# Performance work log

Measured on AMD Instinct MI355X. Metric: run time of the kernel, lower is better.

Reference implementation:

```python
import jax, jax.numpy as jnp
import numpy as np

B, Q, C, N, H, W = 2, 4096, 256, 6, 64, 96
HEADS, POINTS = 8, 4


def _grid_sample(img, grid):
    # img: [G, C, H, W]; grid: [G, P, 2] in [-1,1]
    # bilinear, align_corners=False, padding_mode='zeros' (matches F.grid_sample)
    G, Cc, Hh, Ww = img.shape
    gx = (grid[..., 0] + 1.0) * (Ww / 2.0) - 0.5
    gy = (grid[..., 1] + 1.0) * (Hh / 2.0) - 0.5
    x0f = jnp.floor(gx)
    y0f = jnp.floor(gy)
    wx = (gx - x0f)[:, None, :]
    wy = (gy - y0f)[:, None, :]
    x0 = x0f.astype(jnp.int32)
    y0 = y0f.astype(jnp.int32)
    flat = img.reshape(G, Cc, Hh * Ww)

    def gather(xi, yi):
        valid = ((xi >= 0) & (xi < Ww) & (yi >= 0) & (yi < Hh))
        idx = jnp.clip(yi, 0, Hh - 1) * Ww + jnp.clip(xi, 0, Ww - 1)
        v = jnp.take_along_axis(flat, idx[:, None, :], axis=2)  # [G,C,P]
        return v * valid[:, None, :].astype(img.dtype)

    v00 = gather(x0, y0)
    v01 = gather(x0 + 1, y0)
    v10 = gather(x0, y0 + 1)
    v11 = gather(x0 + 1, y0 + 1)
    return (v00 * (1 - wx) * (1 - wy) + v01 * wx * (1 - wy)
            + v10 * (1 - wx) * wy + v11 * wx * wy)


def setup_inputs() -> dict:
    key = jax.random.key(0)
    ks = jax.random.split(key, 12)
    query = jax.random.normal(ks[0], (B, Q, C), dtype=jnp.float32)
    query_coords = jax.random.uniform(ks[1], (B, Q, 3), dtype=jnp.float32)
    image_feats = jax.random.normal(ks[2], (B, N, C, H, W), dtype=jnp.float32)
    # realistic f-theta fisheye intrinsics for 1280x1080 images
    Kmat = np.array([[500.0, 0.0, 640.0], [0.0, 500.0, 540.0], [0.0, 0.0, 1.0]], dtype=np.float32)
    intrinsics = jnp.asarray(np.tile(Kmat, (B, N, 1, 1)))
    # inverse extrinsics: identity rotation, cameras 3m behind the voxel volume (cam_z > 0)
    E = np.tile(np.eye(4, dtype=np.float32), (B, N, 1, 1))
    for n in range(N):
        E[:, n, 0, 3] = 0.2 * n - 0.5
        E[:, n, 2, 3] = 3.0
    inv_extrinsics = jnp.asarray(E)
    s = 1.0 / np.sqrt(C)
    W_off = jax.random.normal(ks[3], (C, N * HEADS * POINTS * 2), dtype=jnp.float32) * 0.02
    b_off = jnp.zeros((N * HEADS * POINTS * 2,), dtype=jnp.float32)
    W_attn = jax.random.normal(ks[4], (C, N * HEADS * POINTS), dtype=jnp.float32) * s
    b_attn = jnp.zeros((N * HEADS * POINTS,), dtype=jnp.float32)
    W_val = jax.random.normal(ks[5], (C, C), dtype=jnp.float32) * s
    b_val = jax.random.normal(ks[6], (C,), dtype=jnp.float32) * 0.01
    W_out = jax.random.normal(ks[7], (C, C), dtype=jnp.float32) * s
    b_out = jax.random.normal(ks[8], (C,), dtype=jnp.float32) * 0.01
    return {"query": query, "query_coords": query_coords, "image_feats": image_feats,
            "intrinsics": intrinsics, "inv_extrinsics": inv_extrinsics,
            "W_off": W_off, "b_off": b_off, "W_attn": W_attn, "b_attn": b_attn,
            "W_val": W_val, "b_val": b_val, "W_out": W_out, "b_out": b_out}


def reference(query, query_coords, image_feats, intrinsics, inv_extrinsics,
              W_off, b_off, W_attn, b_attn, W_val, b_val, W_out, b_out):
    Bq, Qq, Cq = query.shape
    _, Nn, _, Hh, Ww = image_feats.shape
    hd = Cq // HEADS
    # ---- reference points: voxel coords -> world -> camera -> f-theta image ----
    xmin, ymin, zmin, xmax, ymax, zmax = -3.6, -3.0, -0.7, 3.6, 3.0, 2.5
    rx = query_coords[..., 0] * (xmax - xmin) + xmin
    ry = query_coords[..., 1] * (ymax - ymin) + ymin
    rz = query_coords[..., 2] * (zmax - zmin) + zmin
    world = jnp.stack([rx, ry, rz, jnp.ones_like(rx)], axis=-1)  # [B,Q,4]
    cam = jnp.einsum('bnij,bqj->bnqi', inv_extrinsics, world)    # [B,N,Q,4]
    cxp, cyp, czp = cam[..., 0], cam[..., 1], cam[..., 2]
    r3d = jnp.sqrt(cxp * cxp + cyp * cyp + 1e-8)
    theta = jnp.arctan2(r3d, czp)
    phi = jnp.arctan2(cyp, cxp)
    fx = intrinsics[:, :, 0, 0][..., None]
    cx0 = intrinsics[:, :, 0, 2][..., None]
    cy0 = intrinsics[:, :, 1, 2][..., None]
    r_img = fx * theta
    u = r_img * jnp.cos(phi) + cx0
    v = r_img * jnp.sin(phi) + cy0
    origH, origW = 1080, 1280
    ref = jnp.stack([2.0 * u / (origW - 1) - 1.0, 2.0 * v / (origH - 1) - 1.0], axis=-1)  # [B,N,Q,2]
    fov = ((czp > 0) & (theta < 1.372)).astype(query.dtype)      # [B,N,Q]
    # ---- offsets + attention weights ----
    offs = jnp.tanh((query @ W_off + b_off).reshape(Bq, Qq, Nn, HEADS, POINTS, 2)) * 0.5
    aw = (query @ W_attn + b_attn).reshape(Bq, Qq, Nn, HEADS, POINTS)
    aw = aw * jnp.transpose(fov, (0, 2, 1))[..., None, None]
    aw = jax.nn.softmax(aw, axis=-1)
    # ---- value projection ----
    val = jnp.einsum('bnchw,cd->bnhwd', image_feats, W_val) + b_val  # [B,N,H,W,C]
    val = val.reshape(Bq, Nn, Hh, Ww, HEADS, hd)
    # ---- sampling locations ----
    locs = ref[:, :, :, None, None, :] + jnp.transpose(offs, (0, 2, 1, 3, 4, 5))  # [B,N,Q,h,p,2]
    v_all = jnp.transpose(val, (0, 1, 4, 5, 2, 3)).reshape(Bq * Nn * HEADS, hd, Hh, Ww)
    locs_all = jnp.transpose(locs, (0, 1, 3, 2, 4, 5)).reshape(Bq * Nn * HEADS, Qq * POINTS, 2)
    sampled = _grid_sample(v_all, locs_all).reshape(Bq, Nn, HEADS, hd, Qq, POINTS)
    sampled = jnp.transpose(sampled, (0, 4, 1, 2, 5, 3))  # [B,Q,N,heads,points,hd]
    weighted = jnp.sum(sampled * aw[..., None], axis=4)   # [B,Q,N,heads,hd]
    out = weighted.sum(axis=2).reshape(Bq, Qq, Cq)
    return out @ W_out + b_out
```

## Files before the change

kernel.cpp:

```cpp
#include <hip/hip_runtime.h>
#include <math.h>

#define Bb 2
#define Qq 4096
#define Cc 256
#define Nn 6
#define Hh 64
#define Ww 96
#define HEADS 8
#define POINTS 4
#define HW (Hh*Ww)
#define BQ (Bb*Qq)

#define WS_VAL   0
#define WS_WTF   9437184
#define WS_WCHF  9469952
#define WS_WCLF  9543680
#define WS_WOTF  9617408
#define WS_LOCS  18874368
#define WS_AW    22020096
#define WS_REFF  23592960
#define WS_WSUM  23740416
#define WS_HIST  24788992
#define WS_BOFF  24793088
#define WS_BIN   24797184
#define WS_PERM  24805376

typedef __attribute__((ext_vector_type(8))) short short8;
typedef __attribute__((ext_vector_type(4))) float f32x4;

__device__ __forceinline__ unsigned short f2bf(float f) {
    union { float f; unsigned u; } v; v.f = f;
    unsigned r = (v.u + 0x7fffu + ((v.u >> 16) & 1u)) >> 16;
    return (unsigned short)r;
}
__device__ __forceinline__ float bf2f(unsigned short h) { return __uint_as_float((unsigned)h << 16); }
__device__ __forceinline__ float bflo(unsigned u) { return __uint_as_float(u << 16); }
__device__ __forceinline__ float bfhi(unsigned u) { return __uint_as_float(u & 0xffff0000u); }
__device__ __forceinline__ unsigned packbf(float a, float b) {
    return (unsigned)f2bf(a) | ((unsigned)f2bf(b) << 16);
}

__global__ void prep_kernel(const float* __restrict__ qc,
                            const float* __restrict__ intr,
                            const float* __restrict__ invE,
                            float* __restrict__ reff,
                            const float* __restrict__ Wv,
                            const float* __restrict__ Wo,
                            const float* __restrict__ Wa,
                            const float* __restrict__ Wu,
                            unsigned short* __restrict__ Wtf,
                            unsigned short* __restrict__ Wchf,
                            unsigned short* __restrict__ Wclf,
                            unsigned short* __restrict__ Wotf) {
    int blk = blockIdx.x;
    int tid = threadIdx.x;
    if (blk < 32) {
        int idx = blk * 256 + tid;
        int b = idx >> 12;
        int q = idx & (Qq - 1);
        float rx = qc[idx*3+0] * 7.2f - 3.6f;
        float ry = qc[idx*3+1] * 6.0f - 3.0f;
        float rz = qc[idx*3+2] * 3.2f - 0.7f;
        for (int n = 0; n < Nn; ++n) {
            const float* E = invE + (b*Nn+n)*16;
            float camx = E[0]*rx + E[1]*ry + E[2]*rz  + E[3];
            float camy = E[4]*rx + E[5]*ry + E[6]*rz  + E[7];
            float camz = E[8]*rx + E[9]*ry + E[10]*rz + E[11];
            const float* K = intr + (b*Nn+n)*9;
            float fx = K[0], cx0 = K[2], cy0 = K[5];
            float r3d   = sqrtf(camx*camx + camy*camy + 1e-8f);
            float theta = atan2f(r3d, camz);
            float phi   = atan2f(camy, camx);
            float r_img = fx * theta;
            float u = r_img * cosf(phi) + cx0;
            float v = r_img * sinf(phi) + cy0;
            int base = ((b*Nn+n)*Qq + q)*3;
            reff[base+0] = 2.0f * u / 1279.0f - 1.0f;
            reff[base+1] = 2.0f * v / 1079.0f - 1.0f;
            reff[base+2] = (camz > 0.0f && theta < 1.372f) ? 1.0f : 0.0f;
        }
        return;
    }
    int idx = (blk - 32) * 256 + tid;
    if (idx < 65536) {
        int s = idx & 7, l = (idx >> 3) & 63, kk = (idx >> 9) & 7, t = idx >> 12;
        int n = t*16 + (l & 15);
        int k = kk*32 + (l >> 4)*8 + s;
        Wtf[idx] = f2bf(Wv[k*256 + n]);
    } else if (idx < 212992) {
        int i2 = idx - 65536;
        int s = i2 & 7, l = (i2 >> 3) & 63, kk = (i2 >> 9) & 7, t = i2 >> 12;
        int n = t*16 + (l & 15);
        int k = kk*32 + (l >> 4)*8 + s;
        float w = (n < 384) ? Wo[k*384 + n] : Wa[k*192 + (n - 384)];
        unsigned short h = f2bf(w);
        Wchf[i2] = h;
        Wclf[i2] = f2bf(w - bf2f(h));
    } else {
        int i3 = idx - 212992;
        int s = i3 & 7, l = (i3 >> 3) & 63, kk = (i3 >> 9) & 7, t = i3 >> 12;
        int n = t*16 + (l & 15);
        int k = kk*32 + (l >> 4)*8 + s;
        Wotf[i3] = f2bf(Wu[k*256 + n]);
    }
}

__global__ void bin_kernel(const float* __restrict__ qc,
                           int* __restrict__ hist, int* __restrict__ bin) {
    int q = blockIdx.x*256 + threadIdx.x;
    float x = qc[q*3+0], y = qc[q*3+1], z = qc[q*3+2];
    int bx = min(15, max(0, (int)(x*16.f)));
    int by = min(15, max(0, (int)(y*16.f)));
    int bz = min(7,  max(0, (int)(z*8.f)));
    int b = q >> 12;
    int bn = ((b*8 + bz)*16 + by)*16 + bx;
    bin[q] = bn;
    atomicAdd(&hist[bn], 1);
}

__global__ void scan_kernel(const int* __restrict__ hist, int* __restrict__ boff) {
    __shared__ int psum[256];
    int t = threadIdx.x;
    int loc[16]; int s = 0;
#pragma unroll
    for (int i = 0; i < 16; ++i) { loc[i] = hist[t*16+i]; s += loc[i]; }
    psum[t] = s;
    __syncthreads();
    for (int off = 1; off < 256; off <<= 1) {
        int v = (t >= off) ? psum[t-off] : 0;
        __syncthreads();
        psum[t] += v;
        __syncthreads();
    }
    int base = (t == 0) ? 0 : psum[t-1];
#pragma unroll
    for (int i = 0; i < 16; ++i) { boff[t*16+i] = base; base += loc[i]; }
}

__global__ void scatter_kernel(const int* __restrict__ bin,
                               int* __restrict__ boff, int* __restrict__ perm) {
    int q = blockIdx.x*256 + threadIdx.x;
    int pos = atomicAdd(&boff[bin[q]], 1);
    perm[pos] = q;
}

__global__ __launch_bounds__(512, 2) void vp_mfma_kernel(const float* __restrict__ feats,
                                                         const unsigned short* __restrict__ Wtf,
                                                         const float* __restrict__ bv,
                                                         unsigned short* __restrict__ val) {
    __shared__ __align__(16) unsigned short As[64 * 272];
    int t = threadIdx.x;
    int pix0 = blockIdx.x * 64;
    int bn = blockIdx.y;
    const float* A = feats + (size_t)bn * Cc * HW + pix0;
    int lane = t & 63, wavei = t >> 6, quad = lane >> 4, l15 = lane & 15;
    {
        int pq = t & 15;
        int oct = t >> 4;
        float va[8][4];
#pragma unroll
        for (int j = 0; j < 8; ++j)
            *(float4*)va[j] = *(const float4*)&A[(size_t)(oct*8 + j)*HW + pq*4];
#pragma unroll
        for (int e = 0; e < 4; ++e) {
            int m = pq*4 + e;
            uint4 pk;
            pk.x = packbf(va[0][e], va[1][e]);
            pk.y = packbf(va[2][e], va[3][e]);
            pk.z = packbf(va[4][e], va[5][e]);
            pk.w = packbf(va[6][e], va[7][e]);
            *(uint4*)&As[m*264 + oct*8] = pk;
        }
    }
    __syncthreads();
    int wm = wavei & 1;
    int wn = wavei >> 1;
    int r0 = wm*32 + l15, r1 = r0 + 16;
    const unsigned short* Wl = Wtf + (size_t)lane * 8;
#define VP_BOFF(nt, kk) ((size_t)(((wn*4 + (nt))*8 + (kk)) << 9))
    f32x4 acc[2][4];
#pragma unroll
    for (int i = 0; i < 2; ++i)
#pragma unroll
        for (int j = 0; j < 4; ++j) acc[i][j] = (f32x4){0.f, 0.f, 0.f, 0.f};
    short8 bA[4], bB[4];
#pragma unroll
    for (int nt = 0; nt < 4; ++nt) bA[nt] = *(const short8*)&Wl[VP_BOFF(nt, 0)];
#pragma unroll
    for (int kk = 0; kk < 8; kk += 2) {
        if (kk + 1 < 8) {
#pragma unroll
            for (int nt = 0; nt < 4; ++nt) bB[nt] = *(const short8*)&Wl[VP_BOFF(nt, kk+1)];
        }
        {
            short8 a0 = *(const short8*)&As[r0*264 + kk*32 + quad*8];
            short8 a1 = *(const short8*)&As[r1*264 + kk*32 + quad*8];
#pragma unroll
            for (int nt = 0; nt < 4; ++nt) {
                acc[0][nt] = __builtin_amdgcn_mfma_f32_16x16x32_bf16(a0, bA[nt], acc[0][nt], 0, 0, 0);
                acc[1][nt] = __builtin_amdgcn_mfma_f32_16x16x32_bf16(a1, bA[nt], acc[1][nt], 0, 0, 0);
            }
        }
        if (kk + 2 < 8) {
#pragma unroll
            for (int nt = 0; nt < 4; ++nt) bA[nt] = *(const short8*)&Wl[VP_BOFF(nt, kk+2)];
        }
        if (kk + 1 < 8) {
            int k1 = kk + 1;
            short8 a0 = *(const short8*)&As[r0*264 + k1*32 + quad*8];
            short8 a1 = *(const short8*)&As[r1*264 + k1*32 + quad*8];
#pragma unroll
            for (int nt = 0; nt < 4; ++nt) {
                acc[0][nt] = __builtin_amdgcn_mfma_f32_16x16x32_bf16(a0, bB[nt], acc[0][nt], 0, 0, 0);
                acc[1][nt] = __builtin_amdgcn_mfma_f32_16x16x32_bf16(a1, bB[nt], acc[1][nt], 0, 0, 0);
            }
        }
    }
    __syncthreads();
#pragma unroll
    for (int nt = 0; nt < 4; ++nt) {
        int n = wn*64 + nt*16 + l15;
        float bias = bv[n];
#pragma unroll
        for (int mt = 0; mt < 2; ++mt) {
#pragma unroll
            for (int r = 0; r < 4; ++r) {
                int mm = wm*32 + mt*16 + quad*4 + r;
                As[mm*272 + n] = f2bf(acc[mt][nt][r] + bias);
            }
        }
    }
    __syncthreads();
#pragma unroll
    for (int i = 0; i < 4; ++i) {
        int flat = wavei*2048 + i*512 + lane*8;
        int pix = flat >> 8, ch = flat & 255;
        int head = ch >> 5, c32 = ch & 31;
        *(uint4*)&val[(((size_t)bn*HEADS + head)*HW + pix0 + pix)*32 + c32] =
            *(const uint4*)&As[pix*272 + ch];
    }
}

__global__ __launch_bounds__(512, 4) void qp_kernel(const float* __restrict__ query,
                                                    const unsigned short* __restrict__ Wchf,
                                                    const unsigned short* __restrict__ Wclf,
                                                    const float* __restrict__ b_off,
                                                    const float* __restrict__ b_attn,
                                                    const float* __restrict__ reff,
                                                    float* __restrict__ locs,
                                                    float* __restrict__ aw) {
    __shared__ __align__(16) unsigned short Ah[32 * 256];
    __shared__ __align__(16) unsigned short Al[32 * 256];
    int t = threadIdx.x;
    int row0 = blockIdx.x * 32;
    int ty = blockIdx.y;
    {
        int row = t & 31;
        int c2 = t >> 5;
        const float* src = query + (size_t)(row0 + row) * 256;
#pragma unroll
        for (int cc = 0; cc < 2; ++cc) {
            int c = c2 * 2 + cc;
            float4 v0 = *(const float4*)&src[c*8 + 0];
            float4 v1 = *(const float4*)&src[c*8 + 4];
            float f[8] = {v0.x, v0.y, v0.z, v0.w, v1.x, v1.y, v1.z, v1.w};
            unsigned short h[8], l[8];
#pragma unroll
            for (int j = 0; j < 8; ++j) {
                h[j] = f2bf(f[j]);
                l[j] = f2bf(f[j] - bf2f(h[j]));
            }
            uint4 ph, pl;
            ph.x = h[0] | ((unsigned)h[1] << 16); ph.y = h[2] | ((unsigned)h[3] << 16);
            ph.z = h[4] | ((unsigned)h[5] << 16); ph.w = h[6] | ((unsigned)h[7] << 16);
            pl.x = l[0] | ((unsigned)l[1] << 16); pl.y = l[2] | ((unsigned)l[3] << 16);
            pl.z = l[4] | ((unsigned)l[5] << 16); pl.w = l[6] | ((unsigned)l[7] << 16);
            int pos = row * 256 + ((c ^ row) << 3);
            *(uint4*)&Ah[pos] = ph;
            *(uint4*)&Al[pos] = pl;
        }
    }
    __syncthreads();
    int wave = t >> 6, lane = t & 63, quad = lane >> 4, l15 = lane & 15;
    int ms = wave & 1;
    int ng = wave >> 1;
    int arow = ms*16 + l15;
    int bq = row0 >> 12;
    int tile0 = ty*12 + ng*3;
    f32x4 acc[3];
#pragma unroll
    for (int i = 0; i < 3; ++i) acc[i] = (f32x4){0.f, 0.f, 0.f, 0.f};

#define QP_FB(i, kk) (((size_t)((tile0 + (i))*8 + (kk)) << 9) + lane*8)

    if (ty < 2) {
        short8 bhA[3], blA[3], bhB[3], blB[3];
#pragma unroll
        for (int i = 0; i < 3; ++i) {
            bhA[i] = *(const short8*)&Wchf[QP_FB(i, 0)];
            blA[i] = *(const short8*)&Wclf[QP_FB(i, 0)];
        }
#pragma unroll
        for (int kk = 0; kk < 8; kk += 2) {
            if (kk + 1 < 8) {
#pragma unroll
                for (int i = 0; i < 3; ++i) {
                    bhB[i] = *(const short8*)&Wchf[QP_FB(i, kk+1)];
                    blB[i] = *(const short8*)&Wclf[QP_FB(i, kk+1)];
                }
            }
            {
                int apos = arow*256 + (((kk*4+quad) ^ arow) << 3);
                short8 a_h = *(const short8*)&Ah[apos];
                short8 a_l = *(const short8*)&Al[apos];
#pragma unroll
                for (int i = 0; i < 3; ++i) {
                    acc[i] = __builtin_amdgcn_mfma_f32_16x16x32_bf16(a_h, bhA[i], acc[i], 0, 0, 0);
                    acc[i] = __builtin_amdgcn_mfma_f32_16x16x32_bf16(a_l, bhA[i], acc[i], 0, 0, 0);
                    acc[i] = __builtin_amdgcn_mfma_f32_16x16x32_bf16(a_h, blA[i], acc[i], 0, 0, 0);
                }
            }
            if (kk + 2 < 8) {
#pragma unroll
                for (int i = 0; i < 3; ++i) {
                    bhA[i] = *(const short8*)&Wchf[QP_FB(i, kk+2)];
                    blA[i] = *(const short8*)&Wclf[QP_FB(i, kk+2)];
                }
            }
            if (kk + 1 < 8) {
                int k1 = kk + 1;
                int apos = arow*256 + (((k1*4+quad) ^ arow) << 3);
                short8 a_h = *(const short8*)&Ah[apos];
                short8 a_l = *(const short8*)&Al[apos];
#pragma unroll
                for (int i = 0; i < 3; ++i) {
                    acc[i] = __builtin_amdgcn_mfma_f32_16x16x32_bf16(a_h, bhB[i], acc[i], 0, 0, 0);
                    acc[i] = __builtin_amdgcn_mfma_f32_16x16x32_bf16(a_l, bhB[i], acc[i], 0, 0, 0);
                    acc[i] = __builtin_amdgcn_mfma_f32_16x16x32_bf16(a_h, blB[i], acc[i], 0, 0, 0);
                }
            }
        }
#pragma unroll
        for (int i = 0; i < 3; ++i) {
            int j = (tile0 + i)*16 + l15;
            int n_cam = j >> 6;
            int xy = j & 1;
            float bias = b_off[j];
#pragma unroll
            for (int r = 0; r < 4; ++r) {
                int q = row0 + ms*16 + quad*4 + r;
                int qq = q & (Qq-1);
                float refv = reff[((bq*Nn + n_cam)*Qq + qq)*3 + xy];
                locs[(size_t)q*384 + j] = refv + tanhf(acc[i][r] + bias) * 0.5f;
            }
        }
    } else {
        short8 bhA[3], bhB[3];
#pragma unroll
        for (int i = 0; i < 3; ++i) bhA[i] = *(const short8*)&Wchf[QP_FB(i, 0)];
#pragma unroll
        for (int kk = 0; kk < 8; kk += 2) {
            if (kk + 1 < 8) {
#pragma unroll
                for (int i = 0; i < 3; ++i) bhB[i] = *(const short8*)&Wchf[QP_FB(i, kk+1)];
            }
            {
                int apos = arow*256 + (((kk*4+quad) ^ arow) << 3);
                short8 a_h = *(const short8*)&Ah[apos];
#pragma unroll
                for (int i = 0; i < 3; ++i)
                    acc[i] = __builtin_amdgcn_mfma_f32_16x16x32_bf16(a_h, bhA[i], acc[i], 0, 0, 0);
            }
            if (kk + 2 < 8) {
#pragma unroll
                for (int i = 0; i < 3; ++i) bhA[i] = *(const short8*)&Wchf[QP_FB(i, kk+2)];
            }
            if (kk + 1 < 8) {
                int k1 = kk + 1;
                int apos = arow*256 + (((k1*4+quad) ^ arow) << 3);
                short8 a_h = *(const short8*)&Ah[apos];
#pragma unroll
                for (int i = 0; i < 3; ++i)
                    acc[i] = __builtin_amdgcn_mfma_f32_16x16x32_bf16(a_h, bhB[i], acc[i], 0, 0, 0);
            }
        }
#pragma unroll
        for (int i = 0; i < 3; ++i) {
            int j2 = (tile0 + i)*16 + l15 - 384;
            int n_cam = j2 >> 5;
            float bias = b_attn[j2];
#pragma unroll
            for (int r = 0; r < 4; ++r) {
                int q = row0 + ms*16 + quad*4 + r;
                int qq = q & (Qq-1);
                float fov = reff[((bq*Nn + n_cam)*Qq + qq)*3 + 2];
                float lg = (acc[i][r] + bias) * fov;
                float mx = fmaxf(lg, __shfl_xor(lg, 1));
                mx = fmaxf(mx, __shfl_xor(mx, 2));
                float e = expf(lg - mx);
                float s = e + __shfl_xor(e, 1);
                s = s + __shfl_xor(s, 2);
                aw[(size_t)q*192 + j2] = e / s;
            }
        }
    }
#undef QP_FB
}

__global__ __launch_bounds__(512, 4) void samp_kernel(const unsigned short* __restrict__ val,
                                                      const float* __restrict__ locs,
                                                      const float* __restrict__ aw,
                                                      const int* __restrict__ perm,
                                                      unsigned short* __restrict__ wsum) {
    __shared__ float swgt[8][4][196];
    __shared__ int   soff[8][4][196];
    int t = threadIdx.x, wv = t >> 6, lane = t & 63;
    int bi = blockIdx.x;
    int q = perm[(bi & 7) * 1024 + (bi >> 3) * 8 + wv];
    int b = q >> 12;
#pragma unroll
    for (int j = 0; j < 3; ++j) {
        int s = lane + 64*j;
        float2 xy = *(const float2*)&locs[(size_t)q*384 + 2*s];
        float w = aw[(size_t)q*192 + s];
        float gx = (xy.x + 1.0f)*48.0f - 0.5f;
        float gy = (xy.y + 1.0f)*32.0f - 0.5f;
        float x0f = floorf(gx), y0f = floorf(gy);
        float wx = gx - x0f, wy = gy - y0f;
        int ix = (int)x0f, iy = (int)y0f;
        bool vx0 = (unsigned)ix       < (unsigned)Ww;
        bool vx1 = (unsigned)(ix + 1) < (unsigned)Ww;
        bool vy0 = (unsigned)iy       < (unsigned)Hh;
        bool vy1 = (unsigned)(iy + 1) < (unsigned)Hh;
        int ix0 = min(max(ix, 0), Ww-1), ix1 = min(max(ix+1, 0), Ww-1);
        int iy0 = min(max(iy, 0), Hh-1), iy1 = min(max(iy+1, 0), Hh-1);
        swgt[wv][0][s] = (vx0 && vy0) ? w*(1.0f-wx)*(1.0f-wy) : 0.0f;
        swgt[wv][1][s] = (vx1 && vy0) ? w*wx*(1.0f-wy)        : 0.0f;
        swgt[wv][2][s] = (vx0 && vy1) ? w*(1.0f-wx)*wy        : 0.0f;
        swgt[wv][3][s] = (vx1 && vy1) ? w*wx*wy               : 0.0f;
        soff[wv][0][s] = (iy0*Ww + ix0) * 64;
        soff[wv][1][s] = (iy0*Ww + ix1) * 64;
        soff[wv][2][s] = (iy1*Ww + ix0) * 64;
        soff[wv][3][s] = (iy1*Ww + ix1) * 64;
    }
    __syncthreads();
    int cg   = lane >> 5;
    int head = (lane >> 2) & 7;
    int oc   = lane & 3;
    const char* vbase = (const char*)val + (size_t)(b*Nn*HEADS + head)*HW*64 + oc*16;
    float a[8] = {0.f,0.f,0.f,0.f,0.f,0.f,0.f,0.f};
#pragma unroll
    for (int n = 0; n < Nn; ++n) {
        const char* vb = vbase + (size_t)n*HEADS*HW*64;
#pragma unroll
        for (int p = 0; p < POINTS; ++p) {
            int s = (n*HEADS + head)*POINTS + p;
            float w0 = swgt[wv][cg*2+0][s];
            float w1 = swgt[wv][cg*2+1][s];
            int   o0 = soff[wv][cg*2+0][s];
            int   o1 = soff[wv][cg*2+1][s];
            uint4 u0 = *(const uint4*)(vb + o0);
            uint4 u1 = *(const uint4*)(vb + o1);
            a[0] += w0*bflo(u0.x); a[1] += w0*bfhi(u0.x);
            a[2] += w0*bflo(u0.y); a[3] += w0*bfhi(u0.y);
            a[4] += w0*bflo(u0.z); a[5] += w0*bfhi(u0.z);
            a[6] += w0*bflo(u0.w); a[7] += w0*bfhi(u0.w);
            a[0] += w1*bflo(u1.x); a[1] += w1*bfhi(u1.x);
            a[2] += w1*bflo(u1.y); a[3] += w1*bfhi(u1.y);
            a[4] += w1*bflo(u1.z); a[5] += w1*bfhi(u1.z);
            a[6] += w1*bflo(u1.w); a[7] += w1*bfhi(u1.w);
        }
    }
#pragma unroll
    for (int j = 0; j < 8; ++j) a[j] += __shfl_xor(a[j], 32);
    if (cg == 0) {
        int c = head*32 + oc*8;
        uint4 o;
        o.x = packbf(a[0], a[1]);
        o.y = packbf(a[2], a[3]);
        o.z = packbf(a[4], a[5]);
        o.w = packbf(a[6], a[7]);
        *(uint4*)&wsum[(size_t)q*256 + c] = o;
    }
}

__global__ __launch_bounds__(256) void out_mfma_kernel(const unsigned short* __restrict__ wsum,
                                                       const unsigned short* __restrict__ Wotf,
                                                       const float* __restrict__ b_out,
                                                       float* __restrict__ out) {
    int t = threadIdx.x;
    int row0 = blockIdx.x * 64;
    int col0 = blockIdx.y * 128;
    int wave = t >> 6, lane = t & 63, quad = lane >> 4, l15 = lane & 15;
    int wm = wave & 1;
    int wn = wave >> 1;
    f32x4 acc[2][4];
#pragma unroll
    for (int i = 0; i < 2; ++i)
#pragma unroll
        for (int j = 0; j < 4; ++j) acc[i][j] = (f32x4){0.f, 0.f, 0.f, 0.f};
#pragma unroll
    for (int kk = 0; kk < 8; ++kk) {
        short8 a[2];
#pragma unroll
        for (int mt = 0; mt < 2; ++mt)
            a[mt] = *(const short8*)&wsum[(size_t)(row0 + wm*32 + mt*16 + l15)*256 + kk*32 + quad*8];
#pragma unroll
        for (int nt = 0; nt < 4; ++nt) {
            size_t fb = ((size_t)((blockIdx.y*8 + wn*4 + nt)*8 + kk) << 9) + lane*8;
            short8 bfr = *(const short8*)&Wotf[fb];
            acc[0][nt] = __builtin_amdgcn_mfma_f32_16x16x32_bf16(a[0], bfr, acc[0][nt], 0, 0, 0);
            acc[1][nt] = __builtin_amdgcn_mfma_f32_16x16x32_bf16(a[1], bfr, acc[1][nt], 0, 0, 0);
        }
    }
#pragma unroll
    for (int nt = 0; nt < 4; ++nt) {
        int col = col0 + wn*64 + nt*16 + l15;
        float bias = b_out[col];
#pragma unroll
        for (int mt = 0; mt < 2; ++mt) {
#pragma unroll
            for (int r = 0; r < 4; ++r) {
                int q = row0 + wm*32 + mt*16 + quad*4 + r;
                out[(size_t)q*256 + col] = acc[mt][nt][r] + bias;
            }
        }
    }
}

extern "C" void kernel_launch(void* const* d_in, const int* in_sizes, int n_in,
                              void* d_out, int out_size, void* d_ws, size_t ws_size,
                              hipStream_t stream) {
    const float* query  = (const float*)d_in[0];
    const float* qc     = (const float*)d_in[1];
    const float* feats  = (const float*)d_in[2];
    const float* intr   = (const float*)d_in[3];
    const float* invE   = (const float*)d_in[4];
    const float* W_off  = (const float*)d_in[5];
    const float* b_off  = (const float*)d_in[6];
    const float* W_attn = (const float*)d_in[7];
    const float* b_attn = (const float*)d_in[8];
    const float* W_val  = (const float*)d_in[9];
    const float* b_val  = (const float*)d_in[10];
    const float* W_out  = (const float*)d_in[11];
    const float* b_out  = (const float*)d_in[12];
    float* out = (float*)d_out;
    float* ws  = (float*)d_ws;
    unsigned short* val  = (unsigned short*)(ws + WS_VAL);
    unsigned short* Wtf  = (unsigned short*)(ws + WS_WTF);
    unsigned short* Wchf = (unsigned short*)(ws + WS_WCHF);
    unsigned short* Wclf = (unsigned short*)(ws + WS_WCLF);
    unsigned short* Wotf = (unsigned short*)(ws + WS_WOTF);
    float* locs = ws + WS_LOCS;
    float* aw   = ws + WS_AW;
    float* reff = ws + WS_REFF;
    unsigned short* wsum = (unsigned short*)(ws + WS_WSUM);
    int* hist = (int*)(ws + WS_HIST);
    int* boff = (int*)(ws + WS_BOFF);
    int* bin  = (int*)(ws + WS_BIN);
    int* perm = (int*)(ws + WS_PERM);

    hipMemsetAsync(hist, 0, 4096*sizeof(int), stream);
    hipLaunchKernelGGL(bin_kernel, dim3(BQ/256), dim3(256), 0, stream,
                       qc, hist, bin);
    hipLaunchKernelGGL(scan_kernel, dim3(1), dim3(256), 0, stream,
                       hist, boff);
    hipLaunchKernelGGL(scatter_kernel, dim3(BQ/256), dim3(256), 0, stream,
                       bin, boff, perm);
    hipLaunchKernelGGL(prep_kernel, dim3(1120), dim3(256), 0, stream,
                       qc, intr, invE, reff, W_val, W_off, W_attn, W_out,
                       Wtf, Wchf, Wclf, Wotf);
    hipLaunchKernelGGL(vp_mfma_kernel, dim3(HW/64, Bb*Nn), dim3(512), 0, stream,
                       feats, Wtf, b_val, val);
    hipLaunchKernelGGL(qp_kernel, dim3(BQ/32, 3), dim3(512), 0, stream,
                       query, Wchf, Wclf, b_off, b_attn, reff, locs, aw);
    hipLaunchKernelGGL(samp_kernel, dim3(BQ/8), dim3(512), 0, stream,
                       val, locs, aw, perm, wsum);
    hipLaunchKernelGGL(out_mfma_kernel, dim3(BQ/64, 2), dim3(256), 0, stream,
                       wsum, Wotf, b_out, out);
}
```

Before: 229.4 us.

## Fuse binning into prep kernel, serpentine bin order, pack sampling tables

Removes the separate bin_kernel and computes query spatial bins inside prep_kernel, saving one launch. The bin order becomes serpentine (boustrophedon) so that consecutive bins stay spatially adjacent, which should improve cache locality in the sampling gather. In samp_kernel the shared-memory weight and offset tables are packed as float2 and ushort2 pairs, halving the number of LDS reads and the offset storage. The ushort offsets rely on HW=6144 fitting in 16 bits.

```diff
diff --git a/kernel.cpp b/kernel.cpp
--- a/kernel.cpp
+++ b/kernel.cpp
@@ -52,16 +52,29 @@
                             unsigned short* __restrict__ Wtf,
                             unsigned short* __restrict__ Wchf,
                             unsigned short* __restrict__ Wclf,
-                            unsigned short* __restrict__ Wotf) {
+                            unsigned short* __restrict__ Wotf,
+                            int* __restrict__ hist,
+                            int* __restrict__ bin) {
     int blk = blockIdx.x;
     int tid = threadIdx.x;
     if (blk < 32) {
         int idx = blk * 256 + tid;
         int b = idx >> 12;
         int q = idx & (Qq - 1);
-        float rx = qc[idx*3+0] * 7.2f - 3.6f;
-        float ry = qc[idx*3+1] * 6.0f - 3.0f;
-        float rz = qc[idx*3+2] * 3.2f - 0.7f;
+        float qx = qc[idx*3+0], qy = qc[idx*3+1], qz = qc[idx*3+2];
+        {
+            int bx = min(15, max(0, (int)(qx*16.f)));
+            int by = min(15, max(0, (int)(qy*16.f)));
+            int bz = min(7,  max(0, (int)(qz*8.f)));
+            if (bz & 1) by = 15 - by;
+            if (by & 1) bx = 15 - bx;
+            int bn = ((b*8 + bz)*16 + by)*16 + bx;
+            bin[idx] = bn;
+            atomicAdd(&hist[bn], 1);
+        }
+        float rx = qx * 7.2f - 3.6f;
+        float ry = qy * 6.0f - 3.0f;
+        float rz = qz * 3.2f - 0.7f;
         for (int n = 0; n < Nn; ++n) {
             const float* E = invE + (b*Nn+n)*16;
             float camx = E[0]*rx + E[1]*ry + E[2]*rz  + E[3];
@@ -106,19 +119,6 @@
     }
 }
 
-__global__ void bin_kernel(const float* __restrict__ qc,
-                           int* __restrict__ hist, int* __restrict__ bin) {
-    int q = blockIdx.x*256 + threadIdx.x;
-    float x = qc[q*3+0], y = qc[q*3+1], z = qc[q*3+2];
-    int bx = min(15, max(0, (int)(x*16.f)));
-    int by = min(15, max(0, (int)(y*16.f)));
-    int bz = min(7,  max(0, (int)(z*8.f)));
-    int b = q >> 12;
-    int bn = ((b*8 + bz)*16 + by)*16 + bx;
-    bin[q] = bn;
-    atomicAdd(&hist[bn], 1);
-}
-
 __global__ void scan_kernel(const int* __restrict__ hist, int* __restrict__ boff) {
     __shared__ int psum[256];
     int t = threadIdx.x;
@@ -413,8 +413,8 @@
                                                       const float* __restrict__ aw,
                                                       const int* __restrict__ perm,
                                                       unsigned short* __restrict__ wsum) {
-    __shared__ float swgt[8][4][196];
-    __shared__ int   soff[8][4][196];
+    __shared__ __align__(16) float2  swgtp[8][2][196];
+    __shared__ __align__(8)  ushort2 soffp[8][2][196];
     int t = threadIdx.x, wv = t >> 6, lane = t & 63;
     int bi = blockIdx.x;
     int q = perm[(bi & 7) * 1024 + (bi >> 3) * 8 + wv];
@@ -435,14 +435,20 @@
         bool vy1 = (unsigned)(iy + 1) < (unsigned)Hh;
         int ix0 = min(max(ix, 0), Ww-1), ix1 = min(max(ix+1, 0), Ww-1);
         int iy0 = min(max(iy, 0), Hh-1), iy1 = min(max(iy+1, 0), Hh-1);
-        swgt[wv][0][s] = (vx0 && vy0) ? w*(1.0f-wx)*(1.0f-wy) : 0.0f;
-        swgt[wv][1][s] = (vx1 && vy0) ? w*wx*(1.0f-wy)        : 0.0f;
-        swgt[wv][2][s] = (vx0 && vy1) ? w*(1.0f-wx)*wy        : 0.0f;
-        swgt[wv][3][s] = (vx1 && vy1) ? w*wx*wy               : 0.0f;
-        soff[wv][0][s] = (iy0*Ww + ix0) * 64;
-        soff[wv][1][s] = (iy0*Ww + ix1) * 64;
-        soff[wv][2][s] = (iy1*Ww + ix0) * 64;
-        soff[wv][3][s] = (iy1*Ww + ix1) * 64;
+        float2 w0p, w1p;
+        w0p.x = (vx0 && vy0) ? w*(1.0f-wx)*(1.0f-wy) : 0.0f;
+        w0p.y = (vx1 && vy0) ? w*wx*(1.0f-wy)        : 0.0f;
+        w1p.x = (vx0 && vy1) ? w*(1.0f-wx)*wy        : 0.0f;
+        w1p.y = (vx1 && vy1) ? w*wx*wy               : 0.0f;
+        swgtp[wv][0][s] = w0p;
+        swgtp[wv][1][s] = w1p;
+        ushort2 o0p, o1p;
+        o0p.x = (unsigned short)(iy0*Ww + ix0);
+        o0p.y = (unsigned short)(iy0*Ww + ix1);
+        o1p.x = (unsigned short)(iy1*Ww + ix0);
+        o1p.y = (unsigned short)(iy1*Ww + ix1);
+        soffp[wv][0][s] = o0p;
+        soffp[wv][1][s] = o1p;
     }
     __syncthreads();
     int cg   = lane >> 5;
@@ -456,12 +462,11 @@
 #pragma unroll
         for (int p = 0; p < POINTS; ++p) {
             int s = (n*HEADS + head)*POINTS + p;
-            float w0 = swgt[wv][cg*2+0][s];
-            float w1 = swgt[wv][cg*2+1][s];
-            int   o0 = soff[wv][cg*2+0][s];
-            int   o1 = soff[wv][cg*2+1][s];
-            uint4 u0 = *(const uint4*)(vb + o0);
-            uint4 u1 = *(const uint4*)(vb + o1);
+            float2 wp = swgtp[wv][cg][s];
+            ushort2 op = soffp[wv][cg][s];
+            uint4 u0 = *(const uint4*)(vb + (int)op.x * 64);
+            uint4 u1 = *(const uint4*)(vb + (int)op.y * 64);
+            float w0 = wp.x, w1 = wp.y;
             a[0] += w0*bflo(u0.x); a[1] += w0*bfhi(u0.x);
             a[2] += w0*bflo(u0.y); a[3] += w0*bfhi(u0.y);
             a[4] += w0*bflo(u0.z); a[5] += w0*bfhi(u0.z);
@@ -562,15 +567,13 @@
     int* perm = (int*)(ws + WS_PERM);
 
     hipMemsetAsync(hist, 0, 4096*sizeof(int), stream);
-    hipLaunchKernelGGL(bin_kernel, dim3(BQ/256), dim3(256), 0, stream,
-                       qc, hist, bin);
+    hipLaunchKernelGGL(prep_kernel, dim3(1120), dim3(256), 0, stream,
+                       qc, intr, invE, reff, W_val, W_off, W_attn, W_out,
+                       Wtf, Wchf, Wclf, Wotf, hist, bin);
     hipLaunchKernelGGL(scan_kernel, dim3(1), dim3(256), 0, stream,
                        hist, boff);
     hipLaunchKernelGGL(scatter_kernel, dim3(BQ/256), dim3(256), 0, stream,
                        bin, boff, perm);
-    hipLaunchKernelGGL(prep_kernel, dim3(1120), dim3(256), 0, stream,
-                       qc, intr, invE, reff, W_val, W_off, W_attn, W_out,
-                       Wtf, Wchf, Wclf, Wotf);
     hipLaunchKernelGGL(vp_mfma_kernel, dim3(HW/64, Bb*Nn), dim3(512), 0, stream,
                        feats, Wtf, b_val, val);
     hipLaunchKernelGGL(qp_kernel, dim3(BQ/32, 3), dim3(512), 0, stream,
```

Result: no change. 228.2 us (-0.5%).
